# Kernel tuning notes

Measured on AMD Instinct MI355X. Metric: run time of the kernel, lower is better.

## Reference

```python
import jax, jax.numpy as jnp
import numpy as np

EPS = 1e-12  # layer_norm_eps

def gelu_bert(x):
    return 0.5 * x * (1.0 + jax.lax.erf(x / jnp.sqrt(2.0).astype(x.dtype)))

def sym_normalize(A):
    # D^{-1/2} A D^{-1/2} via outer-product scaling (algebraic form of diag matmuls)
    d = A.sum(-1)                      # [B,N] row sums
    dinv = jnp.power(d, -0.5)
    return A * dinv[..., :, None] * dinv[..., None, :]

def layernorm(x, g, b):
    mu = x.mean(-1, keepdims=True)
    var = ((x - mu) ** 2).mean(-1, keepdims=True)
    return (x - mu) * jax.lax.rsqrt(var + EPS) * g + b

def gcn(x, adj, w1, w2):
    x = jax.nn.relu(jnp.matmul(adj, x @ w1))   # [B,N,I]
    x = jax.nn.relu(jnp.matmul(adj, x @ w2))   # [B,N,H]
    return x

def setup_inputs() -> dict:
    B, N, H, I = 8, 1024, 768, 3072
    key = jax.random.key(0)
    ks = jax.random.split(key, 20)
    s = 0.02
    inp = {
        'nodes': jax.random.normal(ks[0], (B, N, H), jnp.float32),
        'graphs': jax.random.uniform(ks[1], (B, 2, N, N), jnp.float32),
        'gcn1_w1': jax.random.normal(ks[2], (H, I), jnp.float32) * s,
        'gcn1_w2': jax.random.normal(ks[3], (I, H), jnp.float32) * s,
        'gcn2_w1': jax.random.normal(ks[4], (H, I), jnp.float32) * s,
        'gcn2_w2': jax.random.normal(ks[5], (I, H), jnp.float32) * s,
        'exp1_w': jax.random.normal(ks[6], (H, I), jnp.float32) * s,
        'exp1_b': jnp.zeros((I,), jnp.float32),
        'col1_w': jax.random.normal(ks[7], (I, H), jnp.float32) * s,
        'col1_b': jnp.zeros((H,), jnp.float32),
        'exp2_w': jax.random.normal(ks[8], (H, I), jnp.float32) * s,
        'exp2_b': jnp.zeros((I,), jnp.float32),
        'col2_w': jax.random.normal(ks[9], (I, H), jnp.float32) * s,
        'col2_b': jnp.zeros((H,), jnp.float32),
        'gate_w': jax.random.normal(ks[10], (4 * H, H), jnp.float32) * s,
        'gate_b': jnp.zeros((H,), jnp.float32),
        'ln1_g': jnp.ones((H,), jnp.float32),
        'ln1_b': jnp.zeros((H,), jnp.float32),
        'ln2_g': jnp.ones((H,), jnp.float32),
        'ln2_b': jnp.zeros((H,), jnp.float32),
    }
    return inp

def reference(nodes, graphs, gcn1_w1, gcn1_w2, gcn2_w1, gcn2_w2,
              exp1_w, exp1_b, col1_w, col1_b, exp2_w, exp2_b, col2_w, col2_b,
              gate_w, gate_b, ln1_g, ln1_b, ln2_g, ln2_b):
    adj1 = sym_normalize(graphs[:, 0])   # [B,N,N]
    adj2 = sym_normalize(graphs[:, 1])
    g1 = gcn(nodes, adj1, gcn1_w1, gcn1_w2)  # [B,N,H]
    g2 = gcn(nodes, adj2, gcn2_w1, gcn2_w2)
    # FFN + residual + LN (dropout = identity at eval)
    g1 = gelu_bert(g1 @ exp1_w + exp1_b) @ col1_w + col1_b
    g1 = layernorm(nodes + g1, ln1_g, ln1_b)
    g2 = gelu_bert(g2 @ exp2_w + exp2_b) @ col2_w + col2_b
    g2 = layernorm(nodes + g2, ln2_g, ln2_b)
    gate_in = jnp.concatenate((g1, g2, g1 + g2, g1 - g2), axis=2)  # [B,N,4H]
    gate = jax.nn.sigmoid(gate_in @ gate_w + gate_b)
    return gate * g1 + (1.0 - gate) * g2
```

## Files before the change

### kernel.cpp

```cpp
#include <hip/hip_runtime.h>
#include <hip/hip_bf16.h>

typedef __bf16 b8v __attribute__((ext_vector_type(8)));
typedef float  f4v __attribute__((ext_vector_type(4)));

#define AS3(p)  ((__attribute__((address_space(3))) void*)(p))
#define AS1C(p) ((const __attribute__((address_space(1))) void*)(p))

template<int EPI, int OBF>
__global__ __launch_bounds__(256) void gemm_bt(
    const __hip_bfloat16* __restrict__ A,  long long sA,
    const __hip_bfloat16* __restrict__ Bt, long long sB,
    void* __restrict__ Cv, long long sC,
    const float* __restrict__ bias0, const float* __restrict__ bias1,
    int N, int K, int bMask)
{
  const int bz = blockIdx.z;
  A  += (long long)bz * sA;
  Bt += (long long)(bz & bMask) * sB;
  const float* __restrict__ bias = (bz & 1) ? bias1 : bias0;

  __shared__ __hip_bfloat16 As[128 * 32];
  __shared__ __hip_bfloat16 Bs[128 * 32];

  const int tid  = threadIdx.x;
  const int lane = tid & 63;
  const int wave = tid >> 6;

  const long long m0 = (long long)blockIdx.x * 128;
  const long long n0 = (long long)blockIdx.y * 128;

  const int r  = tid >> 2;
  const int kc = (tid & 3) ^ ((r >> 2) & 3);
  const __hip_bfloat16* aSrc = A  + (m0 + r) * (long long)K + kc * 8;
  const __hip_bfloat16* bSrc = Bt + (n0 + r) * (long long)K + kc * 8;

  const int wm = (wave & 1) * 64;
  const int wn = (wave >> 1) * 64;
  const int lm = lane & 15;
  const int kq = lane >> 4;

  const int sw   = (lm >> 2) & 3;
  const int aOff = (wm + lm) * 32 + ((kq ^ sw)) * 8;
  const int bOff = (wn + lm) * 32 + ((kq ^ sw)) * 8;

  f4v acc[4][4];
  const f4v fzero = {0.0f, 0.0f, 0.0f, 0.0f};
#pragma unroll
  for (int i = 0; i < 4; i++)
#pragma unroll
    for (int j = 0; j < 4; j++) acc[i][j] = fzero;

  for (int k0 = 0; k0 < K; k0 += 32) {
    __builtin_amdgcn_global_load_lds(AS1C(aSrc),              AS3(As + tid * 8),        16, 0, 0);
    __builtin_amdgcn_global_load_lds(AS1C(aSrc + 64LL * K),   AS3(As + 2048 + tid * 8), 16, 0, 0);
    __builtin_amdgcn_global_load_lds(AS1C(bSrc),              AS3(Bs + tid * 8),        16, 0, 0);
    __builtin_amdgcn_global_load_lds(AS1C(bSrc + 64LL * K),   AS3(Bs + 2048 + tid * 8), 16, 0, 0);
    __syncthreads();

    b8v af[4], bf[4];
#pragma unroll
    for (int i = 0; i < 4; i++) af[i] = *(const b8v*)(As + aOff + i * 16 * 32);
#pragma unroll
    for (int j = 0; j < 4; j++) bf[j] = *(const b8v*)(Bs + bOff + j * 16 * 32);

#pragma unroll
    for (int i = 0; i < 4; i++)
#pragma unroll
      for (int j = 0; j < 4; j++)
        acc[i][j] = __builtin_amdgcn_mfma_f32_16x16x32_bf16(af[i], bf[j], acc[i][j], 0, 0, 0);

    __syncthreads();
    aSrc += 32; bSrc += 32;
  }

#pragma unroll
  for (int i = 0; i < 4; i++) {
#pragma unroll
    for (int j = 0; j < 4; j++) {
#pragma unroll
      for (int rg = 0; rg < 4; rg++) {
        long long row = m0 + wm + i * 16 + kq * 4 + rg;
        long long col = n0 + wn + j * 16 + lm;
        float v = acc[i][j][rg];
        if constexpr (EPI == 1) v = fmaxf(v, 0.0f);
        if constexpr (EPI == 2) {
          v += bias[col];
          v = 0.5f * v * (1.0f + erff(v * 0.70710678118654752f));
        }
        long long idx = (long long)bz * sC + row * (long long)N + col;
        if constexpr (OBF) ((__hip_bfloat16*)Cv)[idx] = __float2bfloat16(v);
        else               ((float*)Cv)[idx] = v;
      }
    }
  }
}

__global__ __launch_bounds__(256) void rowsum_dinv(const float* __restrict__ g,
                                                   float* __restrict__ dinv)
{
  const int wave = threadIdx.x >> 6, lane = threadIdx.x & 63;
  const long long row = (long long)blockIdx.x * 4 + wave;
  const float4* p = (const float4*)(g + row * 1024);
  float s = 0.0f;
#pragma unroll
  for (int k = 0; k < 4; k++) {
    float4 v = p[lane + k * 64];
    s += v.x + v.y + v.z + v.w;
  }
#pragma unroll
  for (int o = 32; o > 0; o >>= 1) s += __shfl_down(s, o);
  if (lane == 0) dinv[row] = 1.0f / sqrtf(s);
}

__global__ __launch_bounds__(256) void scale_adj(const float* __restrict__ g,
                                                 const float* __restrict__ dinv,
                                                 __hip_bfloat16* __restrict__ out)
{
  const long long t = (long long)blockIdx.x * 256 + threadIdx.x;
  const long long e = t * 4;
  const int m = (int)(e >> 20);
  const int i = (int)((e >> 10) & 1023);
  const int j = (int)(e & 1023);
  const float4 v  = *(const float4*)(g + e);
  const float  di = dinv[m * 1024 + i];
  const float4 dj = *(const float4*)(dinv + m * 1024 + j);
  const int om = (m & 1) * 8 + (m >> 1);
  union { __hip_bfloat16 h[4]; unsigned long long u; } r;
  r.h[0] = __float2bfloat16(v.x * di * dj.x);
  r.h[1] = __float2bfloat16(v.y * di * dj.y);
  r.h[2] = __float2bfloat16(v.z * di * dj.z);
  r.h[3] = __float2bfloat16(v.w * di * dj.w);
  *(unsigned long long*)(out + ((long long)om << 20) + (long long)i * 1024 + j) = r.u;
}

template<typename TIN>
__global__ void transpose_conv(const TIN* __restrict__ in, __hip_bfloat16* __restrict__ out,
                               int R, int C, long long sIn, long long sOut)
{
  __shared__ __hip_bfloat16 tile[32][33];
  in  += (long long)blockIdx.z * sIn;
  out += (long long)blockIdx.z * sOut;
  const int c0 = blockIdx.x * 32, r0 = blockIdx.y * 32;
  const int tx = threadIdx.x, ty = threadIdx.y;
#pragma unroll
  for (int i = 0; i < 32; i += 8)
    tile[ty + i][tx] = __float2bfloat16((float)in[(long long)(r0 + ty + i) * C + c0 + tx]);
  __syncthreads();
#pragma unroll
  for (int i = 0; i < 32; i += 8)
    out[(long long)(c0 + ty + i) * R + r0 + tx] = tile[tx][ty + i];
}

__global__ __launch_bounds__(256) void ln_residual2(
    const float* __restrict__ nodes, const __hip_bfloat16* __restrict__ V,
    const float* __restrict__ colb0, const float* __restrict__ colb1,
    const float* __restrict__ lng0,  const float* __restrict__ lng1,
    const float* __restrict__ lnb0,  const float* __restrict__ lnb1,
    __hip_bfloat16* __restrict__ gcat)
{
  const long long row = blockIdx.x;
  const int g = (int)(row >> 13);
  const long long rr = row & 8191;
  const float* __restrict__ colb = g ? colb1 : colb0;
  const float* __restrict__ lng  = g ? lng1  : lng0;
  const float* __restrict__ lnb  = g ? lnb1  : lnb0;
  const int t = threadIdx.x;
  const long long nbase = rr * 768;
  const long long vbase = row * 768;
  float x[3]; float s = 0.0f, ss = 0.0f;
#pragma unroll
  for (int i = 0; i < 3; i++) {
    const int c = t + i * 256;
    const float v = nodes[nbase + c] + __bfloat162float(V[vbase + c]) + colb[c];
    x[i] = v; s += v; ss += v * v;
  }
  __shared__ float red[8];
#pragma unroll
  for (int o = 32; o > 0; o >>= 1) { s += __shfl_down(s, o); ss += __shfl_down(ss, o); }
  const int wave = t >> 6, lane = t & 63;
  if (lane == 0) { red[wave] = s; red[4 + wave] = ss; }
  __syncthreads();
  if (t == 0) {
    red[0] = red[0] + red[1] + red[2] + red[3];
    red[4] = red[4] + red[5] + red[6] + red[7];
  }
  __syncthreads();
  const float mu  = red[0] * (1.0f / 768.0f);
  float var = red[4] * (1.0f / 768.0f) - mu * mu;
  var = fmaxf(var, 0.0f);
  const float rs = rsqrtf(var + 1e-12f);
#pragma unroll
  for (int i = 0; i < 3; i++) {
    const int c = t + i * 256;
    const float y = (x[i] - mu) * rs * lng[c] + lnb[c];
    gcat[rr * 1536 + g * 768 + c] = __float2bfloat16(y);
  }
}

__global__ __launch_bounds__(256) void build_wefft(const float* __restrict__ gw,
                                                   __hip_bfloat16* __restrict__ wt)
{
  const int idx = blockIdx.x * 256 + threadIdx.x;
  const int n = idx / 1536, k = idx % 1536;
  float v;
  if (k < 768) v = gw[k * 768 + n] + gw[(1536 + k) * 768 + n] + gw[(2304 + k) * 768 + n];
  else {
    const int kk = k - 768;
    v = gw[(768 + kk) * 768 + n] + gw[(1536 + kk) * 768 + n] - gw[(2304 + kk) * 768 + n];
  }
  wt[idx] = __float2bfloat16(v);
}

__global__ __launch_bounds__(256) void final_gate(
    const float* __restrict__ logits, const float* __restrict__ gb,
    const __hip_bfloat16* __restrict__ gcat, float* __restrict__ out)
{
  const unsigned int t = blockIdx.x * 256u + threadIdx.x;
  const unsigned int row = t / 192u;
  const unsigned int col = (t % 192u) * 4u;
  const long long e = (long long)row * 768 + col;
  const float4 L = *(const float4*)(logits + e);
  const float4 B = *(const float4*)(gb + col);
  union { __hip_bfloat16 h[4]; unsigned long long u; } g1, g2;
  g1.u = *(const unsigned long long*)(gcat + (long long)row * 1536 + col);
  g2.u = *(const unsigned long long*)(gcat + (long long)row * 1536 + 768 + col);
  float4 o;
  {
    float a = __bfloat162float(g1.h[0]), b = __bfloat162float(g2.h[0]);
    float s = 1.0f / (1.0f + expf(-(L.x + B.x))); o.x = s * a + (1.0f - s) * b;
  }
  {
    float a = __bfloat162float(g1.h[1]), b = __bfloat162float(g2.h[1]);
    float s = 1.0f / (1.0f + expf(-(L.y + B.y))); o.y = s * a + (1.0f - s) * b;
  }
  {
    float a = __bfloat162float(g1.h[2]), b = __bfloat162float(g2.h[2]);
    float s = 1.0f / (1.0f + expf(-(L.z + B.z))); o.z = s * a + (1.0f - s) * b;
  }
  {
    float a = __bfloat162float(g1.h[3]), b = __bfloat162float(g2.h[3]);
    float s = 1.0f / (1.0f + expf(-(L.w + B.w))); o.w = s * a + (1.0f - s) * b;
  }
  *(float4*)(out + e) = o;
}

extern "C" void kernel_launch(void* const* d_in, const int* in_sizes, int n_in,
                              void* d_out, int out_size, void* d_ws, size_t ws_size,
                              hipStream_t stream)
{
  const float* nodes  = (const float*)d_in[0];
  const float* graphs = (const float*)d_in[1];
  const float* gcn_w1[2] = { (const float*)d_in[2], (const float*)d_in[4] };
  const float* gcn_w2[2] = { (const float*)d_in[3], (const float*)d_in[5] };
  const float* exp_w[2]  = { (const float*)d_in[6],  (const float*)d_in[10] };
  const float* exp_b[2]  = { (const float*)d_in[7],  (const float*)d_in[11] };
  const float* col_w[2]  = { (const float*)d_in[8],  (const float*)d_in[12] };
  const float* col_b[2]  = { (const float*)d_in[9],  (const float*)d_in[13] };
  const float* gate_w = (const float*)d_in[14];
  const float* gate_b = (const float*)d_in[15];
  const float* ln_g[2] = { (const float*)d_in[16], (const float*)d_in[18] };
  const float* ln_b[2] = { (const float*)d_in[17], (const float*)d_in[19] };
  float* out = (float*)d_out;

  char* w = (char*)d_ws;
  auto alloc = [&](size_t bytes) { char* p = w; w += (bytes + 255) & ~(size_t)255; return p; };
  float*          dinv   = (float*)alloc(16384ULL * 4);
  char*           regA   = alloc(16ULL * 1024 * 1024 * 2);
  __hip_bfloat16* adj2   = (__hip_bfloat16*)regA;
  __hip_bfloat16* Gcat   = (__hip_bfloat16*)regA;
  __hip_bfloat16* wefft  = (__hip_bfloat16*)alloc(768ULL * 1536 * 2);
  __hip_bfloat16* bufA2  = (__hip_bfloat16*)alloc(16ULL * 1024 * 768 * 2);
  char*           regD   = alloc(16ULL * 1024 * 768 * 2);
  __hip_bfloat16* Xt     = (__hip_bfloat16*)regD;
  __hip_bfloat16* bufB2  = (__hip_bfloat16*)regD;
  char*           regE   = alloc(2ULL * 8192 * 3072 * 2);
  __hip_bfloat16* X12    = (__hip_bfloat16*)regE;
  float*          logits = (float*)regE;
  __hip_bfloat16* wgt1   = (__hip_bfloat16*)alloc(2ULL * 3072 * 768 * 2);
  __hip_bfloat16* wgt2   = (__hip_bfloat16*)alloc(2ULL * 768 * 3072 * 2);

  const long long sW1 = 3072LL * 768;
  const long long sW2 = 768LL * 3072;
  const long long sNM = 1024LL * 768;
  const long long sBig = 8192LL * 3072;

  rowsum_dinv<<<4096, 256, 0, stream>>>(graphs, dinv);
  transpose_conv<float><<<dim3(24, 32, 8), dim3(32, 8), 0, stream>>>(
      nodes, Xt, 1024, 768, 1024LL * 768, 768LL * 1024);
  build_wefft<<<4608, 256, 0, stream>>>(gate_w, wefft);
  scale_adj<<<16384, 256, 0, stream>>>(graphs, dinv, adj2);
  for (int g = 0; g < 2; g++) {
    transpose_conv<float><<<dim3(96, 24, 1), dim3(32, 8), 0, stream>>>(
        gcn_w1[g], wgt1 + g * sW1, 768, 3072, 0, 0);
    transpose_conv<float><<<dim3(24, 96, 1), dim3(32, 8), 0, stream>>>(
        gcn_w2[g], wgt2 + g * sW2, 3072, 768, 0, 0);
  }

  gemm_bt<0, 1><<<dim3(8, 6, 16), 256, 0, stream>>>(
      adj2, 1LL << 20, Xt, 768LL * 1024, bufA2, sNM, nullptr, nullptr, 768, 1024, 7);
  gemm_bt<1, 1><<<dim3(64, 24, 2), 256, 0, stream>>>(
      bufA2, 8192LL * 768, wgt1, sW1, X12, sBig, nullptr, nullptr, 3072, 768, -1);
  gemm_bt<0, 1><<<dim3(64, 6, 2), 256, 0, stream>>>(
      X12, sBig, wgt2, sW2, bufB2, 8192LL * 768, nullptr, nullptr, 768, 3072, -1);
  for (int g = 0; g < 2; g++) {
    transpose_conv<float><<<dim3(96, 24, 1), dim3(32, 8), 0, stream>>>(
        exp_w[g], wgt1 + g * sW1, 768, 3072, 0, 0);
    transpose_conv<float><<<dim3(24, 96, 1), dim3(32, 8), 0, stream>>>(
        col_w[g], wgt2 + g * sW2, 3072, 768, 0, 0);
  }
  transpose_conv<__hip_bfloat16><<<dim3(24, 32, 16), dim3(32, 8), 0, stream>>>(
      bufB2, bufA2, 1024, 768, 1024LL * 768, 768LL * 1024);
  gemm_bt<1, 1><<<dim3(8, 6, 16), 256, 0, stream>>>(
      adj2, 1LL << 20, bufA2, 768LL * 1024, bufB2, sNM, nullptr, nullptr, 768, 1024, -1);
  gemm_bt<2, 1><<<dim3(64, 24, 2), 256, 0, stream>>>(
      bufB2, 8192LL * 768, wgt1, sW1, X12, sBig, exp_b[0], exp_b[1], 3072, 768, -1);
  gemm_bt<0, 1><<<dim3(64, 6, 2), 256, 0, stream>>>(
      X12, sBig, wgt2, sW2, bufA2, 8192LL * 768, nullptr, nullptr, 768, 3072, -1);
  ln_residual2<<<16384, 256, 0, stream>>>(
      nodes, bufA2, col_b[0], col_b[1], ln_g[0], ln_g[1], ln_b[0], ln_b[1], Gcat);
  gemm_bt<0, 0><<<dim3(64, 6, 1), 256, 0, stream>>>(
      Gcat, 0, wefft, 0, logits, 0, nullptr, nullptr, 768, 1536, -1);
  final_gate<<<6144, 256, 0, stream>>>(logits, gate_b, Gcat, out);
}
```

Before: 865.6 us.

## Vectorize GEMM epilogue via swapped MFMA, fuse gate, drop intermediate transpose

Adds an orientation template parameter. By swapping the MFMA operands, each lane holds four consecutive output columns and can write them with one vector store, and the GEMM gains a transposed-output mode. The GCN second projection now writes its result transposed, so the separate bf16 transpose kernel before the second adjacency GEMM is removed. The sigmoid gate blend is fused into the final GEMM epilogue, which removes the fp32 logits buffer and the final_gate kernel. In exchange, the transposed store path writes with a large stride (8192 elements between rows), which may cost more than the contiguous stores it replaces.

```diff
diff --git a/kernel.cpp b/kernel.cpp
--- a/kernel.cpp
+++ b/kernel.cpp
@@ -3,21 +3,22 @@
 
 typedef __bf16 b8v __attribute__((ext_vector_type(8)));
 typedef float  f4v __attribute__((ext_vector_type(4)));
+typedef unsigned long long ull;
 
 #define AS3(p)  ((__attribute__((address_space(3))) void*)(p))
 #define AS1C(p) ((const __attribute__((address_space(1))) void*)(p))
 
-template<int EPI, int OBF>
+template<int EPI, int OBF, int ORIENT>
 __global__ __launch_bounds__(256) void gemm_bt(
     const __hip_bfloat16* __restrict__ A,  long long sA,
-    const __hip_bfloat16* __restrict__ Bt, long long sB,
-    void* __restrict__ Cv, long long sC,
+    const __hip_bfloat16* __restrict__ Bt, long long sBg, long long sBb, int ldB,
+    void* __restrict__ Cv, long long sC, int ldC,
     const float* __restrict__ bias0, const float* __restrict__ bias1,
-    int N, int K, int bMask)
+    const __hip_bfloat16* __restrict__ gcat, int K)
 {
   const int bz = blockIdx.z;
   A  += (long long)bz * sA;
-  Bt += (long long)(bz & bMask) * sB;
+  Bt += (long long)(bz >> 3) * sBg + (long long)(bz & 7) * sBb;
   const float* __restrict__ bias = (bz & 1) ? bias1 : bias0;
 
   __shared__ __hip_bfloat16 As[128 * 32];
@@ -32,8 +33,8 @@
 
   const int r  = tid >> 2;
   const int kc = (tid & 3) ^ ((r >> 2) & 3);
-  const __hip_bfloat16* aSrc = A  + (m0 + r) * (long long)K + kc * 8;
-  const __hip_bfloat16* bSrc = Bt + (n0 + r) * (long long)K + kc * 8;
+  const __hip_bfloat16* aSrc = A  + (m0 + r) * (long long)K   + kc * 8;
+  const __hip_bfloat16* bSrc = Bt + (n0 + r) * (long long)ldB + kc * 8;
 
   const int wm = (wave & 1) * 64;
   const int wn = (wave >> 1) * 64;
@@ -41,8 +42,8 @@
   const int kq = lane >> 4;
 
   const int sw   = (lm >> 2) & 3;
-  const int aOff = (wm + lm) * 32 + ((kq ^ sw)) * 8;
-  const int bOff = (wn + lm) * 32 + ((kq ^ sw)) * 8;
+  const int aOff = (wm + lm) * 32 + (kq ^ sw) * 8;
+  const int bOff = (wn + lm) * 32 + (kq ^ sw) * 8;
 
   f4v acc[4][4];
   const f4v fzero = {0.0f, 0.0f, 0.0f, 0.0f};
@@ -52,10 +53,10 @@
     for (int j = 0; j < 4; j++) acc[i][j] = fzero;
 
   for (int k0 = 0; k0 < K; k0 += 32) {
-    __builtin_amdgcn_global_load_lds(AS1C(aSrc),              AS3(As + tid * 8),        16, 0, 0);
-    __builtin_amdgcn_global_load_lds(AS1C(aSrc + 64LL * K),   AS3(As + 2048 + tid * 8), 16, 0, 0);
-    __builtin_amdgcn_global_load_lds(AS1C(bSrc),              AS3(Bs + tid * 8),        16, 0, 0);
-    __builtin_amdgcn_global_load_lds(AS1C(bSrc + 64LL * K),   AS3(Bs + 2048 + tid * 8), 16, 0, 0);
+    __builtin_amdgcn_global_load_lds(AS1C(aSrc),                AS3(As + tid * 8),        16, 0, 0);
+    __builtin_amdgcn_global_load_lds(AS1C(aSrc + 64LL * K),     AS3(As + 2048 + tid * 8), 16, 0, 0);
+    __builtin_amdgcn_global_load_lds(AS1C(bSrc),                AS3(Bs + tid * 8),        16, 0, 0);
+    __builtin_amdgcn_global_load_lds(AS1C(bSrc + 64LL * ldB),   AS3(Bs + 2048 + tid * 8), 16, 0, 0);
     __syncthreads();
 
     b8v af[4], bf[4];
@@ -67,30 +68,82 @@
 #pragma unroll
     for (int i = 0; i < 4; i++)
 #pragma unroll
-      for (int j = 0; j < 4; j++)
-        acc[i][j] = __builtin_amdgcn_mfma_f32_16x16x32_bf16(af[i], bf[j], acc[i][j], 0, 0, 0);
+      for (int j = 0; j < 4; j++) {
+        if constexpr (ORIENT == 0)
+          acc[i][j] = __builtin_amdgcn_mfma_f32_16x16x32_bf16(bf[j], af[i], acc[i][j], 0, 0, 0);
+        else
+          acc[i][j] = __builtin_amdgcn_mfma_f32_16x16x32_bf16(af[i], bf[j], acc[i][j], 0, 0, 0);
+      }
 
     __syncthreads();
     aSrc += 32; bSrc += 32;
   }
 
+  char* Cb = (char*)Cv;
+
 #pragma unroll
   for (int i = 0; i < 4; i++) {
 #pragma unroll
     for (int j = 0; j < 4; j++) {
-#pragma unroll
-      for (int rg = 0; rg < 4; rg++) {
-        long long row = m0 + wm + i * 16 + kq * 4 + rg;
-        long long col = n0 + wn + j * 16 + lm;
-        float v = acc[i][j][rg];
-        if constexpr (EPI == 1) v = fmaxf(v, 0.0f);
+      float v[4];
+#pragma unroll
+      for (int rg = 0; rg < 4; rg++) v[rg] = acc[i][j][rg];
+
+      if constexpr (ORIENT == 0) {
+        const long long row  = m0 + wm + i * 16 + lm;
+        const int       colb = (int)n0 + wn + j * 16 + kq * 4;
+        if constexpr (EPI == 1) {
+#pragma unroll
+          for (int rg = 0; rg < 4; rg++) v[rg] = fmaxf(v[rg], 0.0f);
+        }
         if constexpr (EPI == 2) {
-          v += bias[col];
-          v = 0.5f * v * (1.0f + erff(v * 0.70710678118654752f));
-        }
-        long long idx = (long long)bz * sC + row * (long long)N + col;
-        if constexpr (OBF) ((__hip_bfloat16*)Cv)[idx] = __float2bfloat16(v);
-        else               ((float*)Cv)[idx] = v;
+          const float4 b4 = *(const float4*)(bias + colb);
+          const float* bb = (const float*)&b4;
+#pragma unroll
+          for (int rg = 0; rg < 4; rg++) {
+            float x = v[rg] + bb[rg];
+            v[rg] = 0.5f * x * (1.0f + erff(x * 0.70710678118654752f));
+          }
+        }
+        const long long base = bz * sC + row * (long long)ldC + colb;
+        if constexpr (EPI == 3) {
+          const float4 b4 = *(const float4*)(bias0 + colb);
+          const float* bb = (const float*)&b4;
+          union { __hip_bfloat16 h[4]; ull u; } g1, g2;
+          g1.u = *(const ull*)(gcat + row * 1536 + colb);
+          g2.u = *(const ull*)(gcat + row * 1536 + 768 + colb);
+          float o[4];
+#pragma unroll
+          for (int rg = 0; rg < 4; rg++) {
+            const float s = 1.0f / (1.0f + expf(-(v[rg] + bb[rg])));
+            o[rg] = s * __bfloat162float(g1.h[rg]) +
+                    (1.0f - s) * __bfloat162float(g2.h[rg]);
+          }
+          *(float4*)(Cb + base * 4) = *(const float4*)o;
+        } else if constexpr (OBF) {
+          union { __hip_bfloat16 h[4]; ull u; } P;
+#pragma unroll
+          for (int rg = 0; rg < 4; rg++) P.h[rg] = __float2bfloat16(v[rg]);
+          *(ull*)(Cb + base * 2) = P.u;
+        } else {
+          *(float4*)(Cb + base * 4) = *(const float4*)v;
+        }
+      } else {
+        const long long crow = n0 + wn + j * 16 + lm;
+        const long long mb   = m0 + wm + i * 16 + kq * 4;
+        if constexpr (EPI == 1) {
+#pragma unroll
+          for (int rg = 0; rg < 4; rg++) v[rg] = fmaxf(v[rg], 0.0f);
+        }
+        const long long base = bz * sC + crow * (long long)ldC + mb;
+        if constexpr (OBF) {
+          union { __hip_bfloat16 h[4]; ull u; } P;
+#pragma unroll
+          for (int rg = 0; rg < 4; rg++) P.h[rg] = __float2bfloat16(v[rg]);
+          *(ull*)(Cb + base * 2) = P.u;
+        } else {
+          *(float4*)(Cb + base * 4) = *(const float4*)v;
+        }
       }
     }
   }
@@ -126,12 +179,12 @@
   const float  di = dinv[m * 1024 + i];
   const float4 dj = *(const float4*)(dinv + m * 1024 + j);
   const int om = (m & 1) * 8 + (m >> 1);
-  union { __hip_bfloat16 h[4]; unsigned long long u; } r;
+  union { __hip_bfloat16 h[4]; ull u; } r;
   r.h[0] = __float2bfloat16(v.x * di * dj.x);
   r.h[1] = __float2bfloat16(v.y * di * dj.y);
   r.h[2] = __float2bfloat16(v.z * di * dj.z);
   r.h[3] = __float2bfloat16(v.w * di * dj.w);
-  *(unsigned long long*)(out + ((long long)om << 20) + (long long)i * 1024 + j) = r.u;
+  *(ull*)(out + ((long long)om << 20) + (long long)i * 1024 + j) = r.u;
 }
 
 template<typename TIN>
@@ -210,39 +263,6 @@
     v = gw[(768 + kk) * 768 + n] + gw[(1536 + kk) * 768 + n] - gw[(2304 + kk) * 768 + n];
   }
   wt[idx] = __float2bfloat16(v);
-}
-
-__global__ __launch_bounds__(256) void final_gate(
-    const float* __restrict__ logits, const float* __restrict__ gb,
-    const __hip_bfloat16* __restrict__ gcat, float* __restrict__ out)
-{
-  const unsigned int t = blockIdx.x * 256u + threadIdx.x;
-  const unsigned int row = t / 192u;
-  const unsigned int col = (t % 192u) * 4u;
-  const long long e = (long long)row * 768 + col;
-  const float4 L = *(const float4*)(logits + e);
-  const float4 B = *(const float4*)(gb + col);
-  union { __hip_bfloat16 h[4]; unsigned long long u; } g1, g2;
-  g1.u = *(const unsigned long long*)(gcat + (long long)row * 1536 + col);
-  g2.u = *(const unsigned long long*)(gcat + (long long)row * 1536 + 768 + col);
-  float4 o;
-  {
-    float a = __bfloat162float(g1.h[0]), b = __bfloat162float(g2.h[0]);
-    float s = 1.0f / (1.0f + expf(-(L.x + B.x))); o.x = s * a + (1.0f - s) * b;
-  }
-  {
-    float a = __bfloat162float(g1.h[1]), b = __bfloat162float(g2.h[1]);
-    float s = 1.0f / (1.0f + expf(-(L.y + B.y))); o.y = s * a + (1.0f - s) * b;
-  }
-  {
-    float a = __bfloat162float(g1.h[2]), b = __bfloat162float(g2.h[2]);
-    float s = 1.0f / (1.0f + expf(-(L.z + B.z))); o.z = s * a + (1.0f - s) * b;
-  }
-  {
-    float a = __bfloat162float(g1.h[3]), b = __bfloat162float(g2.h[3]);
-    float s = 1.0f / (1.0f + expf(-(L.w + B.w))); o.w = s * a + (1.0f - s) * b;
-  }
-  *(float4*)(out + e) = o;
 }
 
 extern "C" void kernel_launch(void* const* d_in, const int* in_sizes, int n_in,
@@ -274,9 +294,7 @@
   char*           regD   = alloc(16ULL * 1024 * 768 * 2);
   __hip_bfloat16* Xt     = (__hip_bfloat16*)regD;
   __hip_bfloat16* bufB2  = (__hip_bfloat16*)regD;
-  char*           regE   = alloc(2ULL * 8192 * 3072 * 2);
-  __hip_bfloat16* X12    = (__hip_bfloat16*)regE;
-  float*          logits = (float*)regE;
+  __hip_bfloat16* X12    = (__hip_bfloat16*)alloc(2ULL * 8192 * 3072 * 2);
   __hip_bfloat16* wgt1   = (__hip_bfloat16*)alloc(2ULL * 3072 * 768 * 2);
   __hip_bfloat16* wgt2   = (__hip_bfloat16*)alloc(2ULL * 768 * 3072 * 2);
 
@@ -297,29 +315,33 @@
         gcn_w2[g], wgt2 + g * sW2, 3072, 768, 0, 0);
   }
 
-  gemm_bt<0, 1><<<dim3(8, 6, 16), 256, 0, stream>>>(
-      adj2, 1LL << 20, Xt, 768LL * 1024, bufA2, sNM, nullptr, nullptr, 768, 1024, 7);
-  gemm_bt<1, 1><<<dim3(64, 24, 2), 256, 0, stream>>>(
-      bufA2, 8192LL * 768, wgt1, sW1, X12, sBig, nullptr, nullptr, 3072, 768, -1);
-  gemm_bt<0, 1><<<dim3(64, 6, 2), 256, 0, stream>>>(
-      X12, sBig, wgt2, sW2, bufB2, 8192LL * 768, nullptr, nullptr, 768, 3072, -1);
+  gemm_bt<0, 1, 0><<<dim3(8, 6, 16), 256, 0, stream>>>(
+      adj2, 1LL << 20, Xt, 0, sNM, 1024, bufA2, sNM, 768,
+      nullptr, nullptr, nullptr, 1024);
+  gemm_bt<1, 1, 0><<<dim3(64, 24, 2), 256, 0, stream>>>(
+      bufA2, 8192LL * 768, wgt1, 0, sW1, 768, X12, sBig, 3072,
+      nullptr, nullptr, nullptr, 768);
+  gemm_bt<0, 1, 1><<<dim3(64, 6, 2), 256, 0, stream>>>(
+      X12, sBig, wgt2, 0, sW2, 3072, bufA2, 768LL * 8192, 8192,
+      nullptr, nullptr, nullptr, 3072);
   for (int g = 0; g < 2; g++) {
     transpose_conv<float><<<dim3(96, 24, 1), dim3(32, 8), 0, stream>>>(
         exp_w[g], wgt1 + g * sW1, 768, 3072, 0, 0);
     transpose_conv<float><<<dim3(24, 96, 1), dim3(32, 8), 0, stream>>>(
         col_w[g], wgt2 + g * sW2, 3072, 768, 0, 0);
   }
-  transpose_conv<__hip_bfloat16><<<dim3(24, 32, 16), dim3(32, 8), 0, stream>>>(
-      bufB2, bufA2, 1024, 768, 1024LL * 768, 768LL * 1024);
-  gemm_bt<1, 1><<<dim3(8, 6, 16), 256, 0, stream>>>(
-      adj2, 1LL << 20, bufA2, 768LL * 1024, bufB2, sNM, nullptr, nullptr, 768, 1024, -1);
-  gemm_bt<2, 1><<<dim3(64, 24, 2), 256, 0, stream>>>(
-      bufB2, 8192LL * 768, wgt1, sW1, X12, sBig, exp_b[0], exp_b[1], 3072, 768, -1);
-  gemm_bt<0, 1><<<dim3(64, 6, 2), 256, 0, stream>>>(
-      X12, sBig, wgt2, sW2, bufA2, 8192LL * 768, nullptr, nullptr, 768, 3072, -1);
+  gemm_bt<1, 1, 0><<<dim3(8, 6, 16), 256, 0, stream>>>(
+      adj2, 1LL << 20, bufA2, 768LL * 8192, 1024, 8192, bufB2, sNM, 768,
+      nullptr, nullptr, nullptr, 1024);
+  gemm_bt<2, 1, 0><<<dim3(64, 24, 2), 256, 0, stream>>>(
+      bufB2, 8192LL * 768, wgt1, 0, sW1, 768, X12, sBig, 3072,
+      exp_b[0], exp_b[1], nullptr, 768);
+  gemm_bt<0, 1, 0><<<dim3(64, 6, 2), 256, 0, stream>>>(
+      X12, sBig, wgt2, 0, sW2, 3072, bufA2, 8192LL * 768, 768,
+      nullptr, nullptr, nullptr, 3072);
   ln_residual2<<<16384, 256, 0, stream>>>(
       nodes, bufA2, col_b[0], col_b[1], ln_g[0], ln_g[1], ln_b[0], ln_b[1], Gcat);
-  gemm_bt<0, 0><<<dim3(64, 6, 1), 256, 0, stream>>>(
-      Gcat, 0, wefft, 0, logits, 0, nullptr, nullptr, 768, 1536, -1);
-  final_gate<<<6144, 256, 0, stream>>>(logits, gate_b, Gcat, out);
-}
+  gemm_bt<3, 0, 0><<<dim3(64, 6, 1), 256, 0, stream>>>(
+      Gcat, 0, wefft, 0, 0, 1536, out, 0, 768,
+      gate_b, nullptr, Gcat, 1536);
+}
```

After: 866.2 us. No clear change (+0.1%).
